# Kernel optimization log

Hardware: AMD Instinct MI355X
Metric: run time of the kernel (lower is better)

The kernel has to match this reference:

```python
import jax, jax.numpy as jnp
import numpy as np

B, T, I, H, O = 4096, 256, 5, 64, 25


def _lstm_layer(x, Wih, Whh, bih, bhh):
    """One LSTM layer, batch_first. x: [B,T,in], Wih: [4H,in], Whh: [4H,H].
    PyTorch gate order: i, f, g, o."""
    b, t, _ = x.shape
    h_dim = Whh.shape[1]
    # Precompute input contribution for all timesteps: [B,T,4H]
    gx = jnp.einsum('bti,gi->btg', x, Wih) + bih + bhh

    def step(carry, g_t):
        h, c = carry
        gates = g_t + h @ Whh.T  # [B,4H]
        i, f, g, o = jnp.split(gates, 4, axis=-1)
        i = jax.nn.sigmoid(i)
        f = jax.nn.sigmoid(f)
        g = jnp.tanh(g)
        o = jax.nn.sigmoid(o)
        c = f * c + i * g
        h = o * jnp.tanh(c)
        return (h, c), h

    h0 = jnp.zeros((b, h_dim), x.dtype)
    (_, _), hs = jax.lax.scan(step, (h0, h0), jnp.swapaxes(gx, 0, 1))  # hs: [T,B,H]
    return jnp.swapaxes(hs, 0, 1)  # [B,T,H]


def setup_inputs() -> dict:
    key = jax.random.key(0)
    ks = jax.random.split(key, 12)
    k = 1.0 / np.sqrt(H)  # torch LSTM/Linear init scale
    u = lambda kk, shp: jax.random.uniform(kk, shp, jnp.float32, -k, k)
    return {
        'x': jax.random.normal(ks[0], (B, T, I), jnp.float32),
        'Wih0': u(ks[1], (4 * H, I)),
        'Whh0': u(ks[2], (4 * H, H)),
        'bih0': u(ks[3], (4 * H,)),
        'bhh0': u(ks[4], (4 * H,)),
        'Wih1': u(ks[5], (4 * H, H)),
        'Whh1': u(ks[6], (4 * H, H)),
        'bih1': u(ks[7], (4 * H,)),
        'bhh1': u(ks[8], (4 * H,)),
        'Wfc': u(ks[9], (O, H)),
        'bfc': u(ks[10], (O,)),
    }


def reference(x, Wih0, Whh0, bih0, bhh0, Wih1, Whh1, bih1, bhh1, Wfc, bfc):
    # 2-layer LSTM (dropout = identity in eval mode)
    h1 = _lstm_layer(x, Wih0, Whh0, bih0, bhh0)   # [B,T,H]
    h2 = _lstm_layer(h1, Wih1, Whh1, bih1, bhh1)  # [B,T,H]
    last = h2[:, -1, :]                            # [B,H]
    out = last @ Wfc.T + bfc                       # [B,25]
    return out.reshape(x.shape[0], 5, 5)
```

## Files before the change

### kernel.cpp

```cpp
#include <hip/hip_runtime.h>


#define TT   256
#define II   5
#define HH   64
#define OO   25
#define MT   8
#define NTHR 512
#define XP   520
#define HSZ  512
#define HF   65

typedef __attribute__((ext_vector_type(8))) short  short8;
typedef __attribute__((ext_vector_type(4))) float  floatx4;

#define MFMA(a, b, c) __builtin_amdgcn_mfma_f32_16x16x32_bf16(a, b, c, 0, 0, 0)

__device__ __forceinline__ float frcp(float x) { return __builtin_amdgcn_rcpf(x); }
__device__ __forceinline__ float fexp2(float x) { return __builtin_amdgcn_exp2f(x); }
__device__ __forceinline__ unsigned short bf16_rne(float f) {
    unsigned int u = __builtin_bit_cast(unsigned int, f);
    u += 0x7FFFu + ((u >> 16) & 1u);
    return (unsigned short)(u >> 16);
}
__device__ __forceinline__ float cell_update(const floatx4& g, float& c) {
    const float gi = frcp(1.f + fexp2(g[0]));
    const float gf = frcp(1.f + fexp2(g[1]));
    const float gz = fmaf(-2.f, frcp(1.f + fexp2(g[2])), 1.f);
    const float go = frcp(1.f + fexp2(g[3]));
    c = fmaf(gf, c, gi * gz);
    const float tc = fmaf(-2.f, frcp(1.f + fexp2(c * 2.885390082f)), 1.f);
    return go * tc;
}

__global__ __attribute__((amdgpu_flat_work_group_size(512, 512),
                          amdgpu_waves_per_eu(4, 4)))
void lstm_mfma13(const float* __restrict__ x,
                 const float* __restrict__ Wih0, const float* __restrict__ Whh0,
                 const float* __restrict__ bih0, const float* __restrict__ bhh0,
                 const float* __restrict__ Wih1, const float* __restrict__ Whh1,
                 const float* __restrict__ bih1, const float* __restrict__ bhh1,
                 const float* __restrict__ Wfc,  const float* __restrict__ bfc,
                 float* __restrict__ out)
{
    __shared__ __align__(16) unsigned short xhi[MT * XP];
    __shared__ __align__(16) unsigned short h1hi[2 * HSZ];
    __shared__ __align__(16) unsigned short h2hi[2 * HSZ];
    __shared__ __align__(16) float          h2f[MT * HF];

    const int tid   = threadIdx.x;
    const int w     = tid >> 6;
    const int lane  = tid & 63;
    const int b8    = lane & 7;
    const int q     = lane >> 4;
    const int sel   = (lane >> 3) & 1;
    const int jmine = 8 * w + 4 * sel + q;
    const int hw_off = w * 64 + b8 * 8 + 4 * sel + q;
    const int ro8    = (q * 8 + b8) * 8;

    short8 A1h[2][2];
    short8 A2h[2][4];
    short8 Axwh[2];
    {
        const int rr = lane & 15;
        const float sc = ((rr & 3) == 2) ? 2.885390082f : -1.442695041f;
        #pragma unroll
        for (int s = 0; s < 2; ++s) {
            const int g = (rr & 3) * 64 + 4 * (2 * w + s) + (rr >> 2);
            #pragma unroll
            for (int c = 0; c < 2; ++c)
                #pragma unroll
                for (int jj = 0; jj < 8; ++jj)
                    A1h[s][c][jj] = (short)bf16_rne(sc * Whh0[g * HH + c * 32 + q * 8 + jj]);
            #pragma unroll
            for (int c = 0; c < 4; ++c)
                #pragma unroll
                for (int jj = 0; jj < 8; ++jj) {
                    const int k = c * 32 + q * 8 + jj;
                    float wv = (k < HH) ? Wih1[g * HH + k] : Whh1[g * HH + (k - HH)];
                    A2h[s][c][jj] = (short)bf16_rne(sc * wv);
                }
            #pragma unroll
            for (int jj = 0; jj < 8; ++jj) {
                const int k = q * 8 + jj;
                Axwh[s][jj] = (k < II) ? (short)bf16_rne(sc * Wih0[g * II + k]) : (short)0;
            }
        }
    }
    float bias1m[4], bias2m[4];
    #pragma unroll
    for (int r = 0; r < 4; ++r) {
        const int g = r * 64 + jmine;
        const float sc = (r == 2) ? 2.885390082f : -1.442695041f;
        bias1m[r] = sc * (bih0[g] + bhh0[g]);
        bias2m[r] = sc * (bih1[g] + bhh1[g]);
    }

    for (int i = tid; i < MT * XP / 2; i += NTHR)
        ((unsigned int*)xhi)[i] = 0u;
    if (tid < HSZ) {
        ((unsigned int*)h1hi)[tid] = 0u;
        ((unsigned int*)h2hi)[tid] = 0u;
    }
    float c1 = 0.f, c2 = 0.f;
    __syncthreads();

    const int blockBase = blockIdx.x * MT;

    auto refill_x = [&](int t0) {
        const int rb = tid >> 6, dt = tid & 63;
        const float* src = x + ((size_t)(blockBase + rb) * TT + t0 + dt) * II;
        unsigned short* ph = xhi + rb * XP + dt * 8;
        #pragma unroll
        for (int ii = 0; ii < II; ++ii)
            ph[ii] = bf16_rne(src[ii]);
    };

    refill_x(0);
    __syncthreads();
    {
        short8 Bxh = *(const short8*)(xhi + b8 * XP);
        const floatx4 z4 = {0.f, 0.f, 0.f, 0.f};
        floatx4 a1t0 = MFMA(Axwh[0], Bxh, z4);
        floatx4 a1t1 = MFMA(Axwh[1], Bxh, z4);
        floatx4 g1;
        #pragma unroll
        for (int r = 0; r < 4; ++r)
            g1[r] = (sel ? a1t1[r] : a1t0[r]) + bias1m[r];
        const float h = cell_update(g1, c1);
        h1hi[0 * HSZ + hw_off] = bf16_rne(h);
    }
    __syncthreads();

    const unsigned short* xptr = xhi + b8 * XP + 8;

#define STEP_BODY(WP, RP)                                                     \
    {                                                                         \
        short8 Bxh  = *(const short8*)(xptr);                                 \
        xptr += 8;                                                            \
        const floatx4 z4 = {0.f, 0.f, 0.f, 0.f};                              \
        floatx4 a1t0 = MFMA(Axwh[0], Bxh, z4);                                \
        floatx4 a1t1 = MFMA(Axwh[1], Bxh, z4);                                \
        short8 H1h0 = *(const short8*)(h1hi + (WP) * HSZ + ro8);              \
        floatx4 a2t0 = MFMA(A2h[0][0], H1h0, z4);                             \
        floatx4 a2t1 = MFMA(A2h[1][0], H1h0, z4);                             \
        a1t0 = MFMA(A1h[0][0], H1h0, a1t0);                                   \
        a1t1 = MFMA(A1h[1][0], H1h0, a1t1);                                   \
        short8 H1h1 = *(const short8*)(h1hi + (WP) * HSZ + 256 + ro8);        \
        a2t0 = MFMA(A2h[0][1], H1h1, a2t0);                                   \
        a2t1 = MFMA(A2h[1][1], H1h1, a2t1);                                   \
        a1t0 = MFMA(A1h[0][1], H1h1, a1t0);                                   \
        a1t1 = MFMA(A1h[1][1], H1h1, a1t1);                                   \
        short8 H2h0 = *(const short8*)(h2hi + (RP) * HSZ + ro8);              \
        a2t0 = MFMA(A2h[0][2], H2h0, a2t0);                                   \
        a2t1 = MFMA(A2h[1][2], H2h0, a2t1);                                   \
        short8 H2h1 = *(const short8*)(h2hi + (RP) * HSZ + 256 + ro8);        \
        a2t0 = MFMA(A2h[0][3], H2h1, a2t0);                                   \
        a2t1 = MFMA(A2h[1][3], H2h1, a2t1);                                   \
        floatx4 g2, g1;                                                       \
        _Pragma("unroll")                                                     \
        for (int r = 0; r < 4; ++r)                                           \
            g2[r] = (sel ? a2t1[r] : a2t0[r]) + bias2m[r];                    \
        _Pragma("unroll")                                                     \
        for (int r = 0; r < 4; ++r)                                           \
            g1[r] = (sel ? a1t1[r] : a1t0[r]) + bias1m[r];                    \
        {                                                                     \
            const float h = cell_update(g2, c2);                              \
            h2hi[(WP) * HSZ + hw_off] = bf16_rne(h);                          \
        }                                                                     \
        {                                                                     \
            const float h = cell_update(g1, c1);                              \
            h1hi[(RP) * HSZ + hw_off] = bf16_rne(h);                          \
        }                                                                     \
        __syncthreads();                                                      \
    }

    for (int i = 0; i < 254; i += 2) {
        STEP_BODY(0, 1)
        if (((i + 2) & 63) == 0) {
            refill_x(i + 2);
            xptr = xhi + b8 * XP;
            __syncthreads();
        }
        STEP_BODY(1, 0)
    }
    STEP_BODY(0, 1)
#undef STEP_BODY

    {
        const floatx4 z4 = {0.f, 0.f, 0.f, 0.f};
        short8 H1h0 = *(const short8*)(h1hi + 1 * HSZ + ro8);
        floatx4 a2t0 = MFMA(A2h[0][0], H1h0, z4);
        floatx4 a2t1 = MFMA(A2h[1][0], H1h0, z4);
        short8 H1h1 = *(const short8*)(h1hi + 1 * HSZ + 256 + ro8);
        a2t0 = MFMA(A2h[0][1], H1h1, a2t0);
        a2t1 = MFMA(A2h[1][1], H1h1, a2t1);
        short8 H2h0 = *(const short8*)(h2hi + 0 * HSZ + ro8);
        a2t0 = MFMA(A2h[0][2], H2h0, a2t0);
        a2t1 = MFMA(A2h[1][2], H2h0, a2t1);
        short8 H2h1 = *(const short8*)(h2hi + 0 * HSZ + 256 + ro8);
        a2t0 = MFMA(A2h[0][3], H2h1, a2t0);
        a2t1 = MFMA(A2h[1][3], H2h1, a2t1);
        floatx4 g2;
        #pragma unroll
        for (int r = 0; r < 4; ++r)
            g2[r] = (sel ? a2t1[r] : a2t0[r]) + bias2m[r];
        const float h = cell_update(g2, c2);
        h2f[b8 * HF + jmine] = h;
    }
    __syncthreads();

    if (tid < MT * OO) {
        const int bb = tid / OO, o = tid - bb * OO;
        float acc = bfc[o];
        const float* wr = Wfc + o * HH;
        const float* hr = h2f + bb * HF;
        #pragma unroll
        for (int j = 0; j < HH; ++j) acc += wr[j] * hr[j];
        out[((size_t)blockIdx.x * MT + bb) * OO + o] = acc;
    }
}

extern "C" void kernel_launch(void* const* d_in, const int* in_sizes, int n_in,
                              void* d_out, int out_size, void* d_ws, size_t ws_size,
                              hipStream_t stream) {
    const float* x    = (const float*)d_in[0];
    const float* Wih0 = (const float*)d_in[1];
    const float* Whh0 = (const float*)d_in[2];
    const float* bih0 = (const float*)d_in[3];
    const float* bhh0 = (const float*)d_in[4];
    const float* Wih1 = (const float*)d_in[5];
    const float* Whh1 = (const float*)d_in[6];
    const float* bih1 = (const float*)d_in[7];
    const float* bhh1 = (const float*)d_in[8];
    const float* Wfc  = (const float*)d_in[9];
    const float* bfc  = (const float*)d_in[10];
    float* out = (float*)d_out;

    dim3 grid(4096 / MT), block(NTHR);
    lstm_mfma13<<<grid, block, 0, stream>>>(x, Wih0, Whh0, bih0, bhh0,
                                            Wih1, Whh1, bih1, bhh1,
                                            Wfc, bfc, out);
}
```

Baseline: 323.9 us.

## Split cell updates by layer across lane halves instead of gate halves

Each lane previously ran two cell updates per step, one for layer 1 and one for layer 2, picking one of two gate tiles by lane. Now half the lanes own layer 1 and half own layer 2, and each lane updates two hidden units of its own layer. Write pointers are precomputed per parity and all LDS loads are hoisted to the start of the step. The waves_per_eu constraint is relaxed to a minimum of 2, which may let the compiler use more registers. The per-lane transcendental work is unchanged, but layer-2 lanes now wait on the longer layer-2 MFMA chain, which may shift the critical path.

```diff
diff --git a/kernel.cpp b/kernel.cpp
--- a/kernel.cpp
+++ b/kernel.cpp
@@ -34,8 +34,8 @@
 }
 
 __global__ __attribute__((amdgpu_flat_work_group_size(512, 512),
-                          amdgpu_waves_per_eu(4, 4)))
-void lstm_mfma13(const float* __restrict__ x,
+                          amdgpu_waves_per_eu(2)))
+void lstm_mfma16(const float* __restrict__ x,
                  const float* __restrict__ Wih0, const float* __restrict__ Whh0,
                  const float* __restrict__ bih0, const float* __restrict__ bhh0,
                  const float* __restrict__ Wih1, const float* __restrict__ Whh1,
@@ -53,10 +53,9 @@
     const int lane  = tid & 63;
     const int b8    = lane & 7;
     const int q     = lane >> 4;
-    const int sel   = (lane >> 3) & 1;
-    const int jmine = 8 * w + 4 * sel + q;
-    const int hw_off = w * 64 + b8 * 8 + 4 * sel + q;
-    const int ro8    = (q * 8 + b8) * 8;
+    const bool isl2 = ((lane >> 3) & 1) != 0;
+    const int hw_base = w * 64 + b8 * 8 + q;
+    const int ro8     = (q * 8 + b8) * 8;
 
     short8 A1h[2][2];
     short8 A2h[2][4];
@@ -66,7 +65,7 @@
         const float sc = ((rr & 3) == 2) ? 2.885390082f : -1.442695041f;
         #pragma unroll
         for (int s = 0; s < 2; ++s) {
-            const int g = (rr & 3) * 64 + 4 * (2 * w + s) + (rr >> 2);
+            const int g = (rr & 3) * 64 + 8 * w + 4 * s + (rr >> 2);
             #pragma unroll
             for (int c = 0; c < 2; ++c)
                 #pragma unroll
@@ -87,13 +86,17 @@
             }
         }
     }
-    float bias1m[4], bias2m[4];
+    float biasm[2][4];
     #pragma unroll
-    for (int r = 0; r < 4; ++r) {
-        const int g = r * 64 + jmine;
-        const float sc = (r == 2) ? 2.885390082f : -1.442695041f;
-        bias1m[r] = sc * (bih0[g] + bhh0[g]);
-        bias2m[r] = sc * (bih1[g] + bhh1[g]);
+    for (int s = 0; s < 2; ++s) {
+        const int jj = 8 * w + 4 * s + q;
+        #pragma unroll
+        for (int r = 0; r < 4; ++r) {
+            const int g = r * 64 + jj;
+            const float sc = (r == 2) ? 2.885390082f : -1.442695041f;
+            biasm[s][r] = isl2 ? sc * (bih1[g] + bhh1[g])
+                               : sc * (bih0[g] + bhh0[g]);
+        }
     }
 
     for (int i = tid; i < MT * XP / 2; i += NTHR)
@@ -102,7 +105,7 @@
         ((unsigned int*)h1hi)[tid] = 0u;
         ((unsigned int*)h2hi)[tid] = 0u;
     }
-    float c1 = 0.f, c2 = 0.f;
+    float cs0 = 0.f, cs1 = 0.f;
     __syncthreads();
 
     const int blockBase = blockIdx.x * MT;
@@ -115,6 +118,9 @@
         for (int ii = 0; ii < II; ++ii)
             ph[ii] = bf16_rne(src[ii]);
     };
+
+    unsigned short* const hpE = (isl2 ? h2hi + 0 * HSZ : h1hi + 1 * HSZ) + hw_base;
+    unsigned short* const hpO = (isl2 ? h2hi + 1 * HSZ : h1hi + 0 * HSZ) + hw_base;
 
     refill_x(0);
     __syncthreads();
@@ -123,90 +129,97 @@
         const floatx4 z4 = {0.f, 0.f, 0.f, 0.f};
         floatx4 a1t0 = MFMA(Axwh[0], Bxh, z4);
         floatx4 a1t1 = MFMA(Axwh[1], Bxh, z4);
-        floatx4 g1;
-        #pragma unroll
-        for (int r = 0; r < 4; ++r)
-            g1[r] = (sel ? a1t1[r] : a1t0[r]) + bias1m[r];
-        const float h = cell_update(g1, c1);
-        h1hi[0 * HSZ + hw_off] = bf16_rne(h);
+        if (!isl2) {
+            floatx4 g0, g1;
+            #pragma unroll
+            for (int r = 0; r < 4; ++r) { g0[r] = a1t0[r] + biasm[0][r];
+                                          g1[r] = a1t1[r] + biasm[1][r]; }
+            const float h0 = cell_update(g0, cs0);
+            h1hi[0 * HSZ + hw_base + 0] = bf16_rne(h0);
+            const float h1v = cell_update(g1, cs1);
+            h1hi[0 * HSZ + hw_base + 4] = bf16_rne(h1v);
+        }
     }
     __syncthreads();
 
     const unsigned short* xptr = xhi + b8 * XP + 8;
 
-#define STEP_BODY(WP, RP)                                                     \
+#define STEP_BODY(WP, RP, HP)                                                 \
     {                                                                         \
+        short8 H1h0 = *(const short8*)(h1hi + (WP) * HSZ + ro8);              \
+        short8 H1h1 = *(const short8*)(h1hi + (WP) * HSZ + 256 + ro8);        \
+        short8 H2h0 = *(const short8*)(h2hi + (RP) * HSZ + ro8);              \
+        short8 H2h1 = *(const short8*)(h2hi + (RP) * HSZ + 256 + ro8);        \
         short8 Bxh  = *(const short8*)(xptr);                                 \
         xptr += 8;                                                            \
         const floatx4 z4 = {0.f, 0.f, 0.f, 0.f};                              \
+        floatx4 a2t0 = MFMA(A2h[0][0], H1h0, z4);                             \
+        floatx4 a2t1 = MFMA(A2h[1][0], H1h0, z4);                             \
+        a2t0 = MFMA(A2h[0][1], H1h1, a2t0);                                   \
+        a2t1 = MFMA(A2h[1][1], H1h1, a2t1);                                   \
+        a2t0 = MFMA(A2h[0][2], H2h0, a2t0);                                   \
+        a2t1 = MFMA(A2h[1][2], H2h0, a2t1);                                   \
+        a2t0 = MFMA(A2h[0][3], H2h1, a2t0);                                   \
+        a2t1 = MFMA(A2h[1][3], H2h1, a2t1);                                   \
         floatx4 a1t0 = MFMA(Axwh[0], Bxh, z4);                                \
         floatx4 a1t1 = MFMA(Axwh[1], Bxh, z4);                                \
-        short8 H1h0 = *(const short8*)(h1hi + (WP) * HSZ + ro8);              \
-        floatx4 a2t0 = MFMA(A2h[0][0], H1h0, z4);                             \
-        floatx4 a2t1 = MFMA(A2h[1][0], H1h0, z4);                             \
         a1t0 = MFMA(A1h[0][0], H1h0, a1t0);                                   \
         a1t1 = MFMA(A1h[1][0], H1h0, a1t1);                                   \
-        short8 H1h1 = *(const short8*)(h1hi + (WP) * HSZ + 256 + ro8);        \
-        a2t0 = MFMA(A2h[0][1], H1h1, a2t0);                                   \
-        a2t1 = MFMA(A2h[1][1], H1h1, a2t1);                                   \
         a1t0 = MFMA(A1h[0][1], H1h1, a1t0);                                   \
         a1t1 = MFMA(A1h[1][1], H1h1, a1t1);                                   \
-        short8 H2h0 = *(const short8*)(h2hi + (RP) * HSZ + ro8);              \
-        a2t0 = MFMA(A2h[0][2], H2h0, a2t0);                                   \
-        a2t1 = MFMA(A2h[1][2], H2h0, a2t1);                                   \
-        short8 H2h1 = *(const short8*)(h2hi + (RP) * HSZ + 256 + ro8);        \
-        a2t0 = MFMA(A2h[0][3], H2h1, a2t0);                                   \
-        a2t1 = MFMA(A2h[1][3], H2h1, a2t1);                                   \
-        floatx4 g2, g1;                                                       \
+        floatx4 g0, g1;                                                       \
         _Pragma("unroll")                                                     \
-        for (int r = 0; r < 4; ++r)                                           \
-            g2[r] = (sel ? a2t1[r] : a2t0[r]) + bias2m[r];                    \
-        _Pragma("unroll")                                                     \
-        for (int r = 0; r < 4; ++r)                                           \
-            g1[r] = (sel ? a1t1[r] : a1t0[r]) + bias1m[r];                    \
-        {                                                                     \
-            const float h = cell_update(g2, c2);                              \
-            h2hi[(WP) * HSZ + hw_off] = bf16_rne(h);                          \
+        for (int r = 0; r < 4; ++r) {                                         \
+            g0[r] = (isl2 ? a2t0[r] : a1t0[r]) + biasm[0][r];                 \
+            g1[r] = (isl2 ? a2t1[r] : a1t1[r]) + biasm[1][r];                 \
         }                                                                     \
         {                                                                     \
-            const float h = cell_update(g1, c1);                              \
-            h1hi[(RP) * HSZ + hw_off] = bf16_rne(h);                          \
+            const float h = cell_update(g0, cs0);                             \
+            (HP)[0] = bf16_rne(h);                                            \
+        }                                                                     \
+        {                                                                     \
+            const float h = cell_update(g1, cs1);                             \
+            (HP)[4] = bf16_rne(h);                                            \
         }                                                                     \
         __syncthreads();                                                      \
     }
 
     for (int i = 0; i < 254; i += 2) {
-        STEP_BODY(0, 1)
+        STEP_BODY(0, 1, hpE)
         if (((i + 2) & 63) == 0) {
             refill_x(i + 2);
             xptr = xhi + b8 * XP;
             __syncthreads();
         }
-        STEP_BODY(1, 0)
-    }
-    STEP_BODY(0, 1)
+        STEP_BODY(1, 0, hpO)
+    }
+    STEP_BODY(0, 1, hpE)
 #undef STEP_BODY
 
     {
         const floatx4 z4 = {0.f, 0.f, 0.f, 0.f};
         short8 H1h0 = *(const short8*)(h1hi + 1 * HSZ + ro8);
+        short8 H1h1 = *(const short8*)(h1hi + 1 * HSZ + 256 + ro8);
+        short8 H2h0 = *(const short8*)(h2hi + 0 * HSZ + ro8);
+        short8 H2h1 = *(const short8*)(h2hi + 0 * HSZ + 256 + ro8);
         floatx4 a2t0 = MFMA(A2h[0][0], H1h0, z4);
         floatx4 a2t1 = MFMA(A2h[1][0], H1h0, z4);
-        short8 H1h1 = *(const short8*)(h1hi + 1 * HSZ + 256 + ro8);
         a2t0 = MFMA(A2h[0][1], H1h1, a2t0);
         a2t1 = MFMA(A2h[1][1], H1h1, a2t1);
-        short8 H2h0 = *(const short8*)(h2hi + 0 * HSZ + ro8);
         a2t0 = MFMA(A2h[0][2], H2h0, a2t0);
         a2t1 = MFMA(A2h[1][2], H2h0, a2t1);
-        short8 H2h1 = *(const short8*)(h2hi + 0 * HSZ + 256 + ro8);
         a2t0 = MFMA(A2h[0][3], H2h1, a2t0);
         a2t1 = MFMA(A2h[1][3], H2h1, a2t1);
-        floatx4 g2;
-        #pragma unroll
-        for (int r = 0; r < 4; ++r)
-            g2[r] = (sel ? a2t1[r] : a2t0[r]) + bias2m[r];
-        const float h = cell_update(g2, c2);
-        h2f[b8 * HF + jmine] = h;
+        if (isl2) {
+            floatx4 g0, g1;
+            #pragma unroll
+            for (int r = 0; r < 4; ++r) { g0[r] = a2t0[r] + biasm[0][r];
+                                          g1[r] = a2t1[r] + biasm[1][r]; }
+            const float h0 = cell_update(g0, cs0);
+            h2f[b8 * HF + 8 * w + q] = h0;
+            const float h1v = cell_update(g1, cs1);
+            h2f[b8 * HF + 8 * w + 4 + q] = h1v;
+        }
     }
     __syncthreads();
 
@@ -238,7 +251,7 @@
     float* out = (float*)d_out;
 
     dim3 grid(4096 / MT), block(NTHR);
-    lstm_mfma13<<<grid, block, 0, stream>>>(x, Wih0, Whh0, bih0, bhh0,
+    lstm_mfma16<<<grid, block, 0, stream>>>(x, Wih0, Whh0, bih0, bhh0,
                                             Wih1, Whh1, bih1, bhh1,
                                             Wfc, bfc, out);
 }
```

Measured after the change: 349.3 us. 7.8% more time.
